# Optimization experiments

Hardware: AMD Instinct MI355X
Metric: run time of the kernel (lower is better)

Reference implementation:

```python
import jax, jax.numpy as jnp
import numpy as np

H = 16
D_MODEL = 1024
D_K = D_MODEL // H
NEG_INF = -1e9


def setup_inputs() -> dict:
    key = jax.random.key(0)
    ks = jax.random.split(key, 11)
    B, S = 4, 2048
    scale = 1.0 / np.sqrt(D_MODEL)
    inp = {
        "query": jax.random.normal(ks[0], (B, S, D_MODEL), jnp.float32),
        "key": jax.random.normal(ks[1], (B, S, D_MODEL), jnp.float32),
        "value": jax.random.normal(ks[2], (B, S, D_MODEL), jnp.float32),
        "Wq": jax.random.normal(ks[3], (D_MODEL, D_MODEL), jnp.float32) * scale,
        "bq": jnp.zeros((D_MODEL,), jnp.float32),
        "Wk": jax.random.normal(ks[4], (D_MODEL, D_MODEL), jnp.float32) * scale,
        "bk": jnp.zeros((D_MODEL,), jnp.float32),
        "Wv": jax.random.normal(ks[5], (D_MODEL, D_MODEL), jnp.float32) * scale,
        "bv": jnp.zeros((D_MODEL,), jnp.float32),
        "Wo": jax.random.normal(ks[6], (D_MODEL, D_MODEL), jnp.float32) * scale,
        "bo": jnp.zeros((D_MODEL,), jnp.float32),
    }
    return inp


def _split_heads(x):
    # [B, S, D] -> [B, H, S, D_K]
    B, S, _ = x.shape
    return x.reshape(B, S, H, D_K).transpose(0, 2, 1, 3)


def reference(query, key, value, Wq, bq, Wk, bk, Wv, bv, Wo, bo):
    # Linear projections (torch Linear: y = x @ W.T + b)
    q = _split_heads(query @ Wq.T + bq)   # [B,H,S,Dk]
    k = _split_heads(key @ Wk.T + bk)
    v = _split_heads(value @ Wv.T + bv)

    S = q.shape[2]
    scores = jnp.einsum("bhqd,bhkd->bhqk", q, k) / jnp.sqrt(jnp.float32(D_K))
    causal = jnp.tril(jnp.ones((S, S), jnp.bool_))  # [S,S]
    scores = jnp.where(causal[None, None], scores, NEG_INF)
    p_attn = jax.nn.softmax(scores, axis=-1)  # dropout p=0.0 (eval)
    x = jnp.einsum("bhqk,bhkd->bhqd", p_attn, v)  # [B,H,S,Dk]
    B = x.shape[0]
    x = x.transpose(0, 2, 1, 3).reshape(B, S, H * D_K)
    return x @ Wo.T + bo
```

## Files before the change

### kernel.cpp

```cpp
#include <hip/hip_runtime.h>
#include <hip/hip_bf16.h>
#include <stdint.h>

#define NH 16
#define SEQ 2048
#define DMODEL 1024
#define DK 64
#define BATCH 4
#define M_TOT 8192

#define LOG2E 1.44269504088896f
#define QSCALE (0.125f * LOG2E)

typedef short v8bf __attribute__((ext_vector_type(8)));
typedef float f32x4 __attribute__((ext_vector_type(4)));

__device__ __forceinline__ unsigned short f2bf(float f) {
  union { float f; unsigned u; } v; v.f = f;
  return (unsigned short)((v.u + 0x7fffu + ((v.u >> 16) & 1u)) >> 16);
}

__device__ __forceinline__ unsigned pack_bf2(float a, float b) {
  return (unsigned)f2bf(a) | ((unsigned)f2bf(b) << 16);
}

__device__ __forceinline__ void async_load16(const void* g, void* l) {
  __builtin_amdgcn_global_load_lds(
      (const __attribute__((address_space(1))) unsigned int*)(uintptr_t)g,
      (__attribute__((address_space(3))) unsigned int*)(unsigned)(uintptr_t)l,
      16, 0, 0);
}

__global__ __launch_bounds__(256)
void cvt_kernel(const float* __restrict__ q, const float* __restrict__ k,
                const float* __restrict__ v,
                const float* __restrict__ wq, const float* __restrict__ wk,
                const float* __restrict__ wv, const float* __restrict__ wo,
                unsigned short* __restrict__ oq, unsigned short* __restrict__ ok,
                unsigned short* __restrict__ ov,
                unsigned short* __restrict__ owq, unsigned short* __restrict__ owk,
                unsigned short* __restrict__ owv, unsigned short* __restrict__ owo)
{
  const size_t XN = (size_t)M_TOT * DMODEL;
  const size_t WN = (size_t)DMODEL * DMODEL;
  const float* s; unsigned short* d; size_t n;
  switch (blockIdx.y) {
    case 0: s = q;  d = oq;  n = XN; break;
    case 1: s = k;  d = ok;  n = XN; break;
    case 2: s = v;  d = ov;  n = XN; break;
    case 3: s = wq; d = owq; n = WN; break;
    case 4: s = wk; d = owk; n = WN; break;
    case 5: s = wv; d = owv; n = WN; break;
    default: s = wo; d = owo; n = WN; break;
  }
  for (size_t i = ((size_t)blockIdx.x * 256 + threadIdx.x) * 8; i < n;
       i += (size_t)gridDim.x * 256 * 8) {
    float4 a = *(const float4*)(s + i);
    float4 b = *(const float4*)(s + i + 4);
    uint4 p = { pack_bf2(a.x, a.y), pack_bf2(a.z, a.w),
                pack_bf2(b.x, b.y), pack_bf2(b.z, b.w) };
    *(uint4*)(d + i) = p;
  }
}

__global__ __launch_bounds__(256, 2)
void proj_bf16_kernel(const unsigned short* __restrict__ Xq,
                      const unsigned short* __restrict__ Xk,
                      const unsigned short* __restrict__ Xv,
                      const unsigned short* __restrict__ Wqc,
                      const unsigned short* __restrict__ Wkc,
                      const unsigned short* __restrict__ Wvc,
                      const float* __restrict__ bq, const float* __restrict__ bk,
                      const float* __restrict__ bv,
                      unsigned short* __restrict__ Qp, unsigned short* __restrict__ Kp,
                      unsigned short* __restrict__ Vp)
{
  const int z = blockIdx.z;
  const unsigned short* A = (z == 0) ? Xq : (z == 1) ? Xk : Xv;
  const unsigned short* W = (z == 0) ? Wqc : (z == 1) ? Wkc : Wvc;
  const float* bias = (z == 0) ? bq : (z == 1) ? bk : bv;
  unsigned short* Out = (z == 0) ? Qp : (z == 1) ? Kp : Vp;
  const float scale = (z == 0) ? QSCALE : 1.0f;

  __shared__ unsigned short As[128 * 64];
  __shared__ unsigned short Bs[128 * 64];

  const int tid  = threadIdx.x;
  const int m0   = blockIdx.x * 128;
  const int n0   = blockIdx.y * 128;
  const int lane = tid & 63;
  const int wave = tid >> 6;
  const int quad = lane >> 4;
  const int l16  = lane & 15;
  const int wm   = (wave >> 1) * 64;
  const int wn   = (wave & 1) * 64;
  const int lrow = lane >> 3;
  const int lcol = lane & 7;

  f32x4 acc[4][4];
#pragma unroll
  for (int i = 0; i < 4; ++i)
#pragma unroll
    for (int j = 0; j < 4; ++j) acc[i][j] = (f32x4){0.f, 0.f, 0.f, 0.f};

  for (int k0 = 0; k0 < DMODEL; k0 += 64) {
#pragma unroll
    for (int i = 0; i < 4; ++i) {
      int row = wave * 32 + i * 8 + lrow;
      int gc = (lcol ^ (row & 7)) * 8;
      async_load16(A + (size_t)(m0 + row) * DMODEL + k0 + gc, &As[(wave * 32 + i * 8) * 64]);
      async_load16(W + (size_t)(n0 + row) * DMODEL + k0 + gc, &Bs[(wave * 32 + i * 8) * 64]);
    }
    __syncthreads();

#pragma unroll
    for (int ks = 0; ks < 2; ++ks) {
      v8bf af[4], bf[4];
#pragma unroll
      for (int i = 0; i < 4; ++i)
        af[i] = *(const v8bf*)&As[(wm + i * 16 + l16) * 64 + ((ks * 4 + quad) ^ (l16 & 7)) * 8];
#pragma unroll
      for (int j = 0; j < 4; ++j)
        bf[j] = *(const v8bf*)&Bs[(wn + j * 16 + l16) * 64 + ((ks * 4 + quad) ^ (l16 & 7)) * 8];
#pragma unroll
      for (int i = 0; i < 4; ++i)
#pragma unroll
        for (int j = 0; j < 4; ++j)
          acc[i][j] = __builtin_amdgcn_mfma_f32_16x16x32_bf16(af[i], bf[j], acc[i][j], 0, 0, 0);
    }
    __syncthreads();
  }

  if (z < 2) {
#pragma unroll
    for (int j = 0; j < 4; ++j) {
      int colg = n0 + wn + j * 16 + l16;
      float bj = bias[colg];
      int h = colg >> 6, d = colg & 63;
#pragma unroll
      for (int i = 0; i < 4; ++i) {
#pragma unroll
        for (int reg = 0; reg < 4; ++reg) {
          int mrow = m0 + wm + i * 16 + quad * 4 + reg;
          int bb = mrow >> 11, ss = mrow & 2047;
          float val = (acc[i][j][reg] + bj) * scale;
          Out[(((size_t)bb * NH + h) * SEQ + ss) * DK + d] = f2bf(val);
        }
      }
    }
  } else {
#pragma unroll
    for (int j = 0; j < 4; ++j) {
      int colg = n0 + wn + j * 16 + l16;
      float bj = bias[colg];
      int h = colg >> 6, d = colg & 63;
#pragma unroll
      for (int i = 0; i < 4; ++i) {
        int mrow = m0 + wm + i * 16 + quad * 4;
        int bb = mrow >> 11, ss = mrow & 2047;
        uint2 pk = { pack_bf2(acc[i][j][0] + bj, acc[i][j][1] + bj),
                     pack_bf2(acc[i][j][2] + bj, acc[i][j][3] + bj) };
        *(uint2*)(Out + (((size_t)bb * NH + h) * DK + d) * SEQ + ss) = pk;
      }
    }
  }
}

__global__ __launch_bounds__(256, 2)
void attn_kernel(const unsigned short* __restrict__ Qp,
                 const unsigned short* __restrict__ Kp,
                 const unsigned short* __restrict__ VTp,
                 unsigned short* __restrict__ Xout)
{
  const int y  = blockIdx.y;
  const int r  = y & 3, jj = y >> 2;
  const int qt = (jj == 0) ? (15 - r) : (jj == 1) ? (8 + r) : (jj == 2) ? (7 - r) : r;
  const int bh = blockIdx.x;
  const int b  = bh >> 4, h = bh & 15;

  const unsigned short* Qb = Qp  + ((size_t)bh * SEQ + qt * 128) * DK;
  const unsigned short* Kb = Kp  + (size_t)bh * SEQ * DK;
  const unsigned short* Vb = VTp + (size_t)bh * DK * SEQ;

  __shared__ unsigned short Ks[2][64 * 64];
  __shared__ unsigned short VTs[2][64 * 64];
  __shared__ unsigned short Ps[4][16 * 64];

  const int tid  = threadIdx.x;
  const int lane = tid & 63, wave = tid >> 6;
  const int quad = lane >> 4, l16 = lane & 15;
  const int row_lo = qt * 128 + wave * 32;

  v8bf qf[2][2];
#pragma unroll
  for (int rf = 0; rf < 2; ++rf)
#pragma unroll
    for (int ks = 0; ks < 2; ++ks)
      qf[rf][ks] = *(const v8bf*)(Qb + (size_t)(wave * 32 + rf * 16 + l16) * DK + ks * 32 + quad * 8);

  float lp[2][4];
  f32x4 o[2][4];
#pragma unroll
  for (int rf = 0; rf < 2; ++rf)
#pragma unroll
    for (int reg = 0; reg < 4; ++reg) lp[rf][reg] = 0.f;
#pragma unroll
  for (int rf = 0; rf < 2; ++rf)
#pragma unroll
    for (int df = 0; df < 4; ++df) o[rf][df] = (f32x4){0.f, 0.f, 0.f, 0.f};

  const int nchunk = 2 * (qt + 1);
  const int lrow = lane >> 3;
  const int lcol = lane & 7;

#pragma unroll
  for (int is = 0; is < 2; ++is) {
    int row = wave * 16 + is * 8 + lrow;
    int cK = ((lcol ^ (row & 7)) * 8);
    async_load16(Kb + (size_t)row * DK + cK, &Ks[0][(wave * 16 + is * 8) * 64]);
    async_load16(Vb + (size_t)row * SEQ + cK, &VTs[0][(wave * 16 + is * 8) * 64]);
  }
  __syncthreads();

  for (int c = 0; c < nchunk; ++c) {
    const int buf = c & 1;
    const int kb  = c * 64;

    if (c + 1 < nchunk) {
      const int kb2 = kb + 64;
#pragma unroll
      for (int is = 0; is < 2; ++is) {
        int row = wave * 16 + is * 8 + lrow;
        int cc = ((lcol ^ (row & 7)) * 8);
        async_load16(Kb + (size_t)(kb2 + row) * DK + cc, &Ks[buf ^ 1][(wave * 16 + is * 8) * 64]);
        async_load16(Vb + (size_t)row * SEQ + kb2 + cc, &VTs[buf ^ 1][(wave * 16 + is * 8) * 64]);
      }
    }

    if (kb <= row_lo + 31) {
      f32x4 s[2][4];
#pragma unroll
      for (int rf = 0; rf < 2; ++rf)
#pragma unroll
        for (int nf = 0; nf < 4; ++nf) s[rf][nf] = (f32x4){0.f, 0.f, 0.f, 0.f};
#pragma unroll
      for (int ks = 0; ks < 2; ++ks)
#pragma unroll
        for (int nf = 0; nf < 4; ++nf) {
          v8bf kf = *(const v8bf*)&Ks[buf][(nf * 16 + l16) * 64 + ((ks * 4 + quad) ^ (l16 & 7)) * 8];
          s[0][nf] = __builtin_amdgcn_mfma_f32_16x16x32_bf16(qf[0][ks], kf, s[0][nf], 0, 0, 0);
          s[1][nf] = __builtin_amdgcn_mfma_f32_16x16x32_bf16(qf[1][ks], kf, s[1][nf], 0, 0, 0);
        }

      if (kb + 63 > row_lo) {
#pragma unroll
        for (int rf = 0; rf < 2; ++rf)
#pragma unroll
          for (int nf = 0; nf < 4; ++nf) {
            int col = kb + nf * 16 + l16;
#pragma unroll
            for (int reg = 0; reg < 4; ++reg)
              if (col > row_lo + rf * 16 + quad * 4 + reg) s[rf][nf][reg] = -1e30f;
          }
      }

#pragma unroll
      for (int rf = 0; rf < 2; ++rf) {
#pragma unroll
        for (int nf = 0; nf < 4; ++nf)
#pragma unroll
          for (int reg = 0; reg < 4; ++reg)
            s[rf][nf][reg] = __builtin_amdgcn_exp2f(s[rf][nf][reg]);
#pragma unroll
        for (int reg = 0; reg < 4; ++reg)
          lp[rf][reg] += (s[rf][0][reg] + s[rf][1][reg]) + (s[rf][2][reg] + s[rf][3][reg]);

#pragma unroll
        for (int nf = 0; nf < 4; ++nf)
#pragma unroll
          for (int reg = 0; reg < 4; ++reg)
            Ps[wave][(quad * 4 + reg) * 64 +
                     (((nf * 2 + (l16 >> 3)) ^ (quad * 2)) * 8) + (l16 & 7)] =
                f2bf(s[rf][nf][reg]);

#pragma unroll
        for (int ks = 0; ks < 2; ++ks) {
          v8bf pf = *(const v8bf*)&Ps[wave][l16 * 64 + (((ks * 4 + quad) ^ ((l16 >> 2) * 2)) * 8)];
#pragma unroll
          for (int df = 0; df < 4; ++df) {
            v8bf vf = *(const v8bf*)&VTs[buf][(df * 16 + l16) * 64 + ((ks * 4 + quad) ^ (l16 & 7)) * 8];
            o[rf][df] = __builtin_amdgcn_mfma_f32_16x16x32_bf16(pf, vf, o[rf][df], 0, 0, 0);
          }
        }
      }
    }
    __syncthreads();
  }

#pragma unroll
  for (int rf = 0; rf < 2; ++rf) {
#pragma unroll
    for (int off = 1; off < 16; off <<= 1)
#pragma unroll
      for (int reg = 0; reg < 4; ++reg) lp[rf][reg] += __shfl_xor(lp[rf][reg], off);
    float inv[4];
#pragma unroll
    for (int reg = 0; reg < 4; ++reg) inv[reg] = 1.0f / lp[rf][reg];
#pragma unroll
    for (int df = 0; df < 4; ++df)
#pragma unroll
      for (int reg = 0; reg < 4; ++reg) {
        int qrow = row_lo + rf * 16 + quad * 4 + reg;
        Xout[(size_t)(b * SEQ + qrow) * DMODEL + h * DK + df * 16 + l16] =
            f2bf(o[rf][df][reg] * inv[reg]);
      }
  }
}

__global__ __launch_bounds__(256, 2)
void oproj_kernel(const unsigned short* __restrict__ Xa,
                  const unsigned short* __restrict__ Woc,
                  const float* __restrict__ bo,
                  float* __restrict__ Out)
{
  __shared__ unsigned short As[128 * 64];
  __shared__ unsigned short Bs[128 * 64];

  const int tid  = threadIdx.x;
  const int m0   = blockIdx.x * 128;
  const int n0   = blockIdx.y * 128;
  const int lane = tid & 63;
  const int wave = tid >> 6;
  const int quad = lane >> 4;
  const int l16  = lane & 15;
  const int wm   = (wave >> 1) * 64;
  const int wn   = (wave & 1) * 64;
  const int lrow = lane >> 3;
  const int lcol = lane & 7;

  f32x4 acc[4][4];
#pragma unroll
  for (int i = 0; i < 4; ++i)
#pragma unroll
    for (int j = 0; j < 4; ++j) acc[i][j] = (f32x4){0.f, 0.f, 0.f, 0.f};

  for (int k0 = 0; k0 < DMODEL; k0 += 64) {
#pragma unroll
    for (int i = 0; i < 4; ++i) {
      int row = wave * 32 + i * 8 + lrow;
      int gc = (lcol ^ (row & 7)) * 8;
      async_load16(Xa  + (size_t)(m0 + row) * DMODEL + k0 + gc, &As[(wave * 32 + i * 8) * 64]);
      async_load16(Woc + (size_t)(n0 + row) * DMODEL + k0 + gc, &Bs[(wave * 32 + i * 8) * 64]);
    }
    __syncthreads();

#pragma unroll
    for (int ks = 0; ks < 2; ++ks) {
      v8bf af[4], bf[4];
#pragma unroll
      for (int i = 0; i < 4; ++i)
        af[i] = *(const v8bf*)&As[(wm + i * 16 + l16) * 64 + ((ks * 4 + quad) ^ (l16 & 7)) * 8];
#pragma unroll
      for (int j = 0; j < 4; ++j)
        bf[j] = *(const v8bf*)&Bs[(wn + j * 16 + l16) * 64 + ((ks * 4 + quad) ^ (l16 & 7)) * 8];
#pragma unroll
      for (int i = 0; i < 4; ++i)
#pragma unroll
        for (int j = 0; j < 4; ++j)
          acc[i][j] = __builtin_amdgcn_mfma_f32_16x16x32_bf16(af[i], bf[j], acc[i][j], 0, 0, 0);
    }
    __syncthreads();
  }

#pragma unroll
  for (int j = 0; j < 4; ++j) {
    int colg = n0 + wn + j * 16 + l16;
    float bj = bo[colg];
#pragma unroll
    for (int i = 0; i < 4; ++i) {
#pragma unroll
      for (int reg = 0; reg < 4; ++reg) {
        int mrow = m0 + wm + i * 16 + quad * 4 + reg;
        Out[(size_t)mrow * DMODEL + colg] = acc[i][j][reg] + bj;
      }
    }
  }
}

extern "C" void kernel_launch(void* const* d_in, const int* in_sizes, int n_in,
                              void* d_out, int out_size, void* d_ws, size_t ws_size,
                              hipStream_t stream)
{
  const float* query = (const float*)d_in[0];
  const float* key   = (const float*)d_in[1];
  const float* value = (const float*)d_in[2];
  const float* Wq = (const float*)d_in[3];
  const float* bq = (const float*)d_in[4];
  const float* Wk = (const float*)d_in[5];
  const float* bk = (const float*)d_in[6];
  const float* Wv = (const float*)d_in[7];
  const float* bv = (const float*)d_in[8];
  const float* Wo = (const float*)d_in[9];
  const float* bo = (const float*)d_in[10];

  const size_t tsz = (size_t)M_TOT * DMODEL;
  const size_t wsz = (size_t)DMODEL * DMODEL;
  unsigned short* Qp  = (unsigned short*)d_ws;
  unsigned short* Kp  = Qp + tsz;
  unsigned short* Vp  = Kp + tsz;
  unsigned short* Xa  = Vp + tsz;
  unsigned short* Xqc = Xa + tsz;
  unsigned short* Xkc = Xqc + tsz;
  unsigned short* Xvc = Xkc + tsz;
  unsigned short* Wqc = Xvc + tsz;
  unsigned short* Wkc = Wqc + wsz;
  unsigned short* Wvc = Wkc + wsz;
  unsigned short* Woc = Wvc + wsz;

  cvt_kernel<<<dim3(1024, 7), 256, 0, stream>>>(query, key, value, Wq, Wk, Wv, Wo,
                                                Xqc, Xkc, Xvc, Wqc, Wkc, Wvc, Woc);
  proj_bf16_kernel<<<dim3(64, 8, 3), 256, 0, stream>>>(Xqc, Xkc, Xvc, Wqc, Wkc, Wvc,
                                                       bq, bk, bv, Qp, Kp, Vp);
  attn_kernel<<<dim3(64, 16), 256, 0, stream>>>(Qp, Kp, Vp, Xa);
  oproj_kernel<<<dim3(64, 8), 256, 0, stream>>>(Xa, Woc, bo, (float*)d_out);
}
```

Measured before the change: 317.2 us.

## Fuse fp32-to-bf16 activation conversion into QKV projection tile loads

The separate conversion pass no longer converts the three fp32 activation tensors; the projection kernel now reads fp32 activations directly from global memory, converts them to bf16 in registers and writes them swizzled into shared memory. This removes a full write and re-read of three bf16 activation copies, and the cvt kernel now handles only the weights. In exchange the A-tile load becomes synchronous register traffic rather than async global-to-LDS, it doubles the bytes read per A tile (fp32), and it adds conversion work and register pressure inside the GEMM loop. The bf16 rounding helpers also switch to the HIP intrinsics.

```diff
diff --git a/kernel.cpp b/kernel.cpp
--- a/kernel.cpp
+++ b/kernel.cpp
@@ -15,13 +15,16 @@
 typedef short v8bf __attribute__((ext_vector_type(8)));
 typedef float f32x4 __attribute__((ext_vector_type(4)));
 
+__device__ __forceinline__ unsigned pack_bf2(float a, float b) {
+  union { __hip_bfloat162 h; unsigned u; } v;
+  v.h = __float22bfloat162_rn(make_float2(a, b));
+  return v.u;
+}
+
 __device__ __forceinline__ unsigned short f2bf(float f) {
-  union { float f; unsigned u; } v; v.f = f;
-  return (unsigned short)((v.u + 0x7fffu + ((v.u >> 16) & 1u)) >> 16);
-}
-
-__device__ __forceinline__ unsigned pack_bf2(float a, float b) {
-  return (unsigned)f2bf(a) | ((unsigned)f2bf(b) << 16);
+  union { __hip_bfloat16 h; unsigned short u; } v;
+  v.h = __float2bfloat16(f);
+  return v.u;
 }
 
 __device__ __forceinline__ void async_load16(const void* g, void* l) {
@@ -32,28 +35,20 @@
 }
 
 __global__ __launch_bounds__(256)
-void cvt_kernel(const float* __restrict__ q, const float* __restrict__ k,
-                const float* __restrict__ v,
-                const float* __restrict__ wq, const float* __restrict__ wk,
+void cvt_kernel(const float* __restrict__ wq, const float* __restrict__ wk,
                 const float* __restrict__ wv, const float* __restrict__ wo,
-                unsigned short* __restrict__ oq, unsigned short* __restrict__ ok,
-                unsigned short* __restrict__ ov,
                 unsigned short* __restrict__ owq, unsigned short* __restrict__ owk,
                 unsigned short* __restrict__ owv, unsigned short* __restrict__ owo)
 {
-  const size_t XN = (size_t)M_TOT * DMODEL;
   const size_t WN = (size_t)DMODEL * DMODEL;
-  const float* s; unsigned short* d; size_t n;
+  const float* s; unsigned short* d;
   switch (blockIdx.y) {
-    case 0: s = q;  d = oq;  n = XN; break;
-    case 1: s = k;  d = ok;  n = XN; break;
-    case 2: s = v;  d = ov;  n = XN; break;
-    case 3: s = wq; d = owq; n = WN; break;
-    case 4: s = wk; d = owk; n = WN; break;
-    case 5: s = wv; d = owv; n = WN; break;
-    default: s = wo; d = owo; n = WN; break;
-  }
-  for (size_t i = ((size_t)blockIdx.x * 256 + threadIdx.x) * 8; i < n;
+    case 0: s = wq; d = owq; break;
+    case 1: s = wk; d = owk; break;
+    case 2: s = wv; d = owv; break;
+    default: s = wo; d = owo; break;
+  }
+  for (size_t i = ((size_t)blockIdx.x * 256 + threadIdx.x) * 8; i < WN;
        i += (size_t)gridDim.x * 256 * 8) {
     float4 a = *(const float4*)(s + i);
     float4 b = *(const float4*)(s + i + 4);
@@ -64,9 +59,9 @@
 }
 
 __global__ __launch_bounds__(256, 2)
-void proj_bf16_kernel(const unsigned short* __restrict__ Xq,
-                      const unsigned short* __restrict__ Xk,
-                      const unsigned short* __restrict__ Xv,
+void proj_bf16_kernel(const float* __restrict__ Xq,
+                      const float* __restrict__ Xk,
+                      const float* __restrict__ Xv,
                       const unsigned short* __restrict__ Wqc,
                       const unsigned short* __restrict__ Wkc,
                       const unsigned short* __restrict__ Wvc,
@@ -76,7 +71,7 @@
                       unsigned short* __restrict__ Vp)
 {
   const int z = blockIdx.z;
-  const unsigned short* A = (z == 0) ? Xq : (z == 1) ? Xk : Xv;
+  const float* A = (z == 0) ? Xq : (z == 1) ? Xk : Xv;
   const unsigned short* W = (z == 0) ? Wqc : (z == 1) ? Wkc : Wvc;
   const float* bias = (z == 0) ? bq : (z == 1) ? bk : bv;
   unsigned short* Out = (z == 0) ? Qp : (z == 1) ? Kp : Vp;
@@ -97,6 +92,9 @@
   const int lrow = lane >> 3;
   const int lcol = lane & 7;
 
+  const int arow8 = tid >> 3;
+  const int au    = tid & 7;
+
   f32x4 acc[4][4];
 #pragma unroll
   for (int i = 0; i < 4; ++i)
@@ -104,12 +102,25 @@
     for (int j = 0; j < 4; ++j) acc[i][j] = (f32x4){0.f, 0.f, 0.f, 0.f};
 
   for (int k0 = 0; k0 < DMODEL; k0 += 64) {
+    float4 av[4][2];
+#pragma unroll
+    for (int g = 0; g < 4; ++g) {
+      const float* src = A + (size_t)(m0 + g * 32 + arow8) * DMODEL + k0 + au * 8;
+      av[g][0] = *(const float4*)src;
+      av[g][1] = *(const float4*)(src + 4);
+    }
 #pragma unroll
     for (int i = 0; i < 4; ++i) {
       int row = wave * 32 + i * 8 + lrow;
       int gc = (lcol ^ (row & 7)) * 8;
-      async_load16(A + (size_t)(m0 + row) * DMODEL + k0 + gc, &As[(wave * 32 + i * 8) * 64]);
       async_load16(W + (size_t)(n0 + row) * DMODEL + k0 + gc, &Bs[(wave * 32 + i * 8) * 64]);
+    }
+#pragma unroll
+    for (int g = 0; g < 4; ++g) {
+      int row = g * 32 + arow8;
+      uint4 p = { pack_bf2(av[g][0].x, av[g][0].y), pack_bf2(av[g][0].z, av[g][0].w),
+                  pack_bf2(av[g][1].x, av[g][1].y), pack_bf2(av[g][1].z, av[g][1].w) };
+      *(uint4*)&As[row * 64 + ((au ^ (row & 7)) * 8)] = p;
     }
     __syncthreads();
 
@@ -409,17 +420,13 @@
   unsigned short* Kp  = Qp + tsz;
   unsigned short* Vp  = Kp + tsz;
   unsigned short* Xa  = Vp + tsz;
-  unsigned short* Xqc = Xa + tsz;
-  unsigned short* Xkc = Xqc + tsz;
-  unsigned short* Xvc = Xkc + tsz;
-  unsigned short* Wqc = Xvc + tsz;
+  unsigned short* Wqc = Xa + tsz;
   unsigned short* Wkc = Wqc + wsz;
   unsigned short* Wvc = Wkc + wsz;
   unsigned short* Woc = Wvc + wsz;
 
-  cvt_kernel<<<dim3(1024, 7), 256, 0, stream>>>(query, key, value, Wq, Wk, Wv, Wo,
-                                                Xqc, Xkc, Xvc, Wqc, Wkc, Wvc, Woc);
-  proj_bf16_kernel<<<dim3(64, 8, 3), 256, 0, stream>>>(Xqc, Xkc, Xvc, Wqc, Wkc, Wvc,
+  cvt_kernel<<<dim3(256, 4), 256, 0, stream>>>(Wq, Wk, Wv, Wo, Wqc, Wkc, Wvc, Woc);
+  proj_bf16_kernel<<<dim3(64, 8, 3), 256, 0, stream>>>(query, key, value, Wqc, Wkc, Wvc,
                                                        bq, bk, bv, Qp, Kp, Vp);
   attn_kernel<<<dim3(64, 16), 256, 0, stream>>>(Qp, Kp, Vp, Xa);
   oproj_kernel<<<dim3(64, 8), 256, 0, stream>>>(Xa, Woc, bo, (float*)d_out);
```

New measurement: 311.6 us. About the same (-1.8%).
